# Performance work log

Measured on AMD Instinct MI355X. Metric: run time of the kernel, lower is better.

The kernel has to match this reference:

```python
import jax, jax.numpy as jnp
import numpy as np

N_NODES = 100000
N_EDGES = 1_600_000
D = 64


def setup_inputs() -> dict:
    key = jax.random.key(0)
    ks = jax.random.split(key, 10)
    features = jax.random.normal(ks[0], (N_NODES, D), dtype=jnp.float32)
    src = jax.random.randint(ks[1], (N_EDGES,), 0, N_NODES, dtype=jnp.int64)
    dst = jax.random.randint(ks[2], (N_EDGES,), 0, N_NODES, dtype=jnp.int64)
    s = 1.0 / np.sqrt(D)
    W0 = jax.random.uniform(ks[3], (D, D), jnp.float32, -s, s)
    b0 = jnp.zeros((D,), jnp.float32)
    W1 = jax.random.uniform(ks[4], (D, D), jnp.float32, -s, s)
    b1 = jnp.zeros((D,), jnp.float32)
    W2 = jax.random.uniform(ks[5], (D, D), jnp.float32, -s, s)
    b2 = jnp.zeros((D,), jnp.float32)
    return {"features": features, "src": src, "dst": dst,
            "W0": W0, "b0": b0, "W1": W1, "b1": b1, "W2": W2, "b2": b2}


def _graph_conv_left(h, src, dst, deg_inv, W, b, act):
    # norm='left': scale source features by 1/out_degree, then copy-sum aggregate
    h = h * deg_inv[:, None]          # [N, d]
    msgs = h[src]                     # [E, d] gather
    agg = jax.ops.segment_sum(msgs, dst, num_segments=N_NODES)  # [N, d]
    out = agg @ W + b
    return act(out) if act is not None else out


def reference(features, src, dst, W0, b0, W1, b1, W2, b2):
    # out-degree with clamp(min=1), as in DGL GraphConv
    deg = jax.ops.segment_sum(jnp.ones((N_EDGES,), jnp.float32), src,
                              num_segments=N_NODES)
    deg_inv = 1.0 / jnp.maximum(deg, 1.0)
    h = _graph_conv_left(features, src, dst, deg_inv, W0, b0, jax.nn.relu)
    h = _graph_conv_left(h, src, dst, deg_inv, W1, b1, jax.nn.relu)
    h = _graph_conv_left(h, src, dst, deg_inv, W2, b2, None)
    mN = jnp.mean(h, axis=0, keepdims=True)  # readout_nodes op='mean', single graph -> [1, d]
    return (h, mN)
```

## Files before the change

### kernel.cpp

```cpp
#include <hip/hip_runtime.h>
#include <hip/hip_fp16.h>

#define D 64
#define NBUK 391
#define NBIN (2 * NBUK)
#define CHUNK 8192
#define PBSTRIDE 256

__global__ __launch_bounds__(256) void phase1_kernel(const int* __restrict__ src,
                                                     const int* __restrict__ dst,
                                                     int* __restrict__ per_block, int E) {
    __shared__ int h[NBIN];
    int tid = (int)threadIdx.x;
    for (int j = tid; j < NBIN; j += 256) h[j] = 0;
    __syncthreads();
    int base = blockIdx.x * CHUNK;
    int cnt = min(CHUNK, E - base);
    for (int k = tid * 4; k < cnt; k += 1024) {
        if (k + 3 < cnt) {
            int4 d4 = *(const int4*)(dst + base + k);
            int4 s4 = *(const int4*)(src + base + k);
            atomicAdd(&h[d4.x >> 8], 1); atomicAdd(&h[d4.y >> 8], 1);
            atomicAdd(&h[d4.z >> 8], 1); atomicAdd(&h[d4.w >> 8], 1);
            atomicAdd(&h[NBUK + (s4.x >> 8)], 1); atomicAdd(&h[NBUK + (s4.y >> 8)], 1);
            atomicAdd(&h[NBUK + (s4.z >> 8)], 1); atomicAdd(&h[NBUK + (s4.w >> 8)], 1);
        } else {
            int kend = (k + 4 < cnt) ? k + 4 : cnt;
            for (int t = k; t < kend; ++t) {
                atomicAdd(&h[dst[base + t] >> 8], 1);
                atomicAdd(&h[NBUK + (src[base + t] >> 8)], 1);
            }
        }
    }
    __syncthreads();
    for (int j = tid; j < NBIN; j += 256) per_block[j * PBSTRIDE + blockIdx.x] = h[j];
}

__global__ __launch_bounds__(256) void scanA_kernel(int* __restrict__ per_block,
                                                    int* __restrict__ total) {
    int wv = (int)threadIdx.x >> 6;
    int lane = (int)threadIdx.x & 63;
    int j = blockIdx.x * 4 + wv;
    if (j >= NBIN) return;
    int* pb = per_block + (size_t)j * PBSTRIDE;
    int4 v = *(const int4*)(pb + lane * 4);
    int s1 = v.x + v.y, s2 = s1 + v.z, s3 = s2 + v.w;
    int x = s3;
#pragma unroll
    for (int d = 1; d < 64; d <<= 1) {
        int t = __shfl_up(x, d);
        if (lane >= d) x += t;
    }
    int excl = x - s3;
    int4 r = make_int4(excl, excl + v.x, excl + s1, excl + s2);
    *(int4*)(pb + lane * 4) = r;
    if (lane == 63) total[j] = x;
}

__global__ __launch_bounds__(512) void scanB_kernel(const int* __restrict__ total,
                                                    int* __restrict__ cb_dst,
                                                    int* __restrict__ cb_src,
                                                    float* __restrict__ msum) {
    __shared__ int s[512];
    int tid = (int)threadIdx.x;
    if (tid < D) msum[tid] = 0.0f;
    for (int half = 0; half < 2; ++half) {
        int v = (tid < NBUK) ? total[half * NBUK + tid] : 0;
        s[tid] = v;
        __syncthreads();
        for (int off = 1; off < 512; off <<= 1) {
            int t = (tid >= off) ? s[tid - off] : 0;
            __syncthreads();
            s[tid] += t;
            __syncthreads();
        }
        int* cb = half ? cb_src : cb_dst;
        if (tid < NBUK) cb[tid] = s[tid] - v;
        if (tid == NBUK - 1) cb[NBUK] = s[tid];
        __syncthreads();
    }
}

__global__ __launch_bounds__(256) void phase2_kernel(const int* __restrict__ src,
                                                     const int* __restrict__ dst,
                                                     const int* __restrict__ per_block,
                                                     const int* __restrict__ cb_dst,
                                                     const int* __restrict__ cb_src,
                                                     int* __restrict__ pairs,
                                                     unsigned char* __restrict__ skeys, int E) {
    __shared__ int lcur[NBIN];
    int tid = (int)threadIdx.x;
    for (int j = tid; j < NBIN; j += 256)
        lcur[j] = per_block[(size_t)j * PBSTRIDE + blockIdx.x] +
                  (j < NBUK ? cb_dst[j] : cb_src[j - NBUK]);
    __syncthreads();
    int base = blockIdx.x * CHUNK;
    int cnt = min(CHUNK, E - base);
    for (int k = tid * 4; k < cnt; k += 1024) {
        if (k + 3 < cnt) {
            int4 d4 = *(const int4*)(dst + base + k);
            int4 s4 = *(const int4*)(src + base + k);
            int p;
            p = atomicAdd(&lcur[d4.x >> 8], 1); pairs[p] = (s4.x << 8) | (d4.x & 255);
            p = atomicAdd(&lcur[d4.y >> 8], 1); pairs[p] = (s4.y << 8) | (d4.y & 255);
            p = atomicAdd(&lcur[d4.z >> 8], 1); pairs[p] = (s4.z << 8) | (d4.z & 255);
            p = atomicAdd(&lcur[d4.w >> 8], 1); pairs[p] = (s4.w << 8) | (d4.w & 255);
            p = atomicAdd(&lcur[NBUK + (s4.x >> 8)], 1); skeys[p] = (unsigned char)(s4.x & 255);
            p = atomicAdd(&lcur[NBUK + (s4.y >> 8)], 1); skeys[p] = (unsigned char)(s4.y & 255);
            p = atomicAdd(&lcur[NBUK + (s4.z >> 8)], 1); skeys[p] = (unsigned char)(s4.z & 255);
            p = atomicAdd(&lcur[NBUK + (s4.w >> 8)], 1); skeys[p] = (unsigned char)(s4.w & 255);
        } else {
            int kend = (k + 4 < cnt) ? k + 4 : cnt;
            for (int t = k; t < kend; ++t) {
                int dv = dst[base + t], sv = src[base + t];
                int p = atomicAdd(&lcur[dv >> 8], 1);
                pairs[p] = (sv << 8) | (dv & 255);
                p = atomicAdd(&lcur[NBUK + (sv >> 8)], 1);
                skeys[p] = (unsigned char)(sv & 255);
            }
        }
    }
}

__global__ __launch_bounds__(256) void finalize_csr_kernel(const int* __restrict__ pairs,
                                                           const unsigned char* __restrict__ skeys,
                                                           const int* __restrict__ cb_dst,
                                                           const int* __restrict__ cb_src,
                                                           const float* __restrict__ feat,
                                                           int* __restrict__ row_ptr,
                                                           int* __restrict__ col,
                                                           float* __restrict__ dinv,
                                                           __half* __restrict__ hs, int N) {
    __shared__ int fine[256];
    __shared__ int lcur[256];
    __shared__ float dsh[256];
    __shared__ int wtot[4], wexcl[4];
    int b = (int)blockIdx.x;
    int tid = (int)threadIdx.x, lane = tid & 63, wv = tid >> 6;
    int g = b * 256 + tid;

    fine[tid] = 0;
    __syncthreads();
    int sb0 = cb_src[b], sb1 = cb_src[b + 1];
    for (int i = sb0 + tid; i < sb1; i += 256) atomicAdd(&fine[skeys[i]], 1);
    __syncthreads();
    float dv_ = 1.0f / fmaxf((float)fine[tid], 1.0f);
    dsh[tid] = dv_;
    if (g < N) dinv[g] = dv_;
    __syncthreads();

    {
        int q = tid & 7;
        int rbase = tid >> 3;
        for (int p = 0; p < 8; ++p) {
            int r = p * 32 + rbase;
            int node = b * 256 + r;
            if (node < N) {
                float sc = dsh[r];
                const float4* f = (const float4*)(feat + (size_t)node * D + q * 8);
                float4 v0 = f[0], v1 = f[1];
                __half2 h[4];
                h[0] = __floats2half2_rn(v0.x * sc, v0.y * sc);
                h[1] = __floats2half2_rn(v0.z * sc, v0.w * sc);
                h[2] = __floats2half2_rn(v1.x * sc, v1.y * sc);
                h[3] = __floats2half2_rn(v1.z * sc, v1.w * sc);
                *(float4*)(hs + (size_t)node * D + q * 8) = *(float4*)h;
            }
        }
    }
    __syncthreads();

    fine[tid] = 0;
    __syncthreads();
    int cb0 = cb_dst[b], cb1 = cb_dst[b + 1];
    for (int i = cb0 + tid; i < cb1; i += 256) atomicAdd(&fine[pairs[i] & 255], 1);
    __syncthreads();
    int v = fine[tid], x = v;
#pragma unroll
    for (int d = 1; d < 64; d <<= 1) {
        int t = __shfl_up(x, d);
        if (lane >= d) x += t;
    }
    if (lane == 63) wtot[wv] = x;
    __syncthreads();
    if (tid == 0) {
        int a = 0;
#pragma unroll
        for (int k = 0; k < 4; ++k) { wexcl[k] = a; a += wtot[k]; }
    }
    __syncthreads();
    int excl = x - v + wexcl[wv];
    if (g <= N) row_ptr[g] = cb0 + excl;
    lcur[tid] = cb0 + excl;
    __syncthreads();
    for (int i = cb0 + tid; i < cb1; i += 256) {
        int p = pairs[i];
        int pos = atomicAdd(&lcur[p & 255], 1);
        col[pos] = p >> 8;
    }
}

__device__ inline void accum8(float* a, float4 raw) {
    __half2* h = (__half2*)&raw;
#pragma unroll
    for (int k = 0; k < 4; ++k) {
        float2 f = __half22float2(h[k]);
        a[2 * k] += f.x;
        a[2 * k + 1] += f.y;
    }
}

__global__ __launch_bounds__(256) void fused_kernel(const __half* __restrict__ hs_in,
                                                    const int* __restrict__ row_ptr,
                                                    const int* __restrict__ col,
                                                    const float* __restrict__ W,
                                                    const float* __restrict__ bias,
                                                    const float* __restrict__ dinv,
                                                    float* __restrict__ outf,
                                                    __half* __restrict__ outh,
                                                    float* __restrict__ msum,
                                                    int N, int mode) {
    int tid = (int)threadIdx.x;
    int lane = tid & 63;
    int wv = tid >> 6;
    int sg = lane >> 3;
    int q = lane & 7;
    int g = wv * 8 + sg;

    float Wreg[64];
#pragma unroll
    for (int k = 0; k < 64; ++k) Wreg[k] = W[k * 64 + lane];
    float breg = bias[lane];

    __shared__ float aggT[32][68];
    float colacc = 0.0f;

    int ntiles = (N + 31) >> 5;
    for (int tile = blockIdx.x; tile < ntiles; tile += gridDim.x) {
        int node_g = tile * 32 + g;
        float a[8];
#pragma unroll
        for (int k = 0; k < 8; ++k) a[k] = 0.0f;
        if (node_g < N) {
            int beg = row_ptr[node_g], end = row_ptr[node_g + 1];
            int j = beg;
            for (; j + 3 < end; j += 4) {
                int s0 = col[j], s1 = col[j + 1], s2 = col[j + 2], s3 = col[j + 3];
                float4 r0 = *(const float4*)(hs_in + (size_t)s0 * D + q * 8);
                float4 r1 = *(const float4*)(hs_in + (size_t)s1 * D + q * 8);
                float4 r2 = *(const float4*)(hs_in + (size_t)s2 * D + q * 8);
                float4 r3 = *(const float4*)(hs_in + (size_t)s3 * D + q * 8);
                accum8(a, r0); accum8(a, r1); accum8(a, r2); accum8(a, r3);
            }
            for (; j < end; ++j) {
                int s0 = col[j];
                float4 r0 = *(const float4*)(hs_in + (size_t)s0 * D + q * 8);
                accum8(a, r0);
            }
        }
        *(float4*)(&aggT[g][q * 8]) = make_float4(a[0], a[1], a[2], a[3]);
        *(float4*)(&aggT[g][q * 8 + 4]) = make_float4(a[4], a[5], a[6], a[7]);

#pragma unroll
        for (int rr = 0; rr < 8; ++rr) {
            int r = wv * 8 + rr;
            int node = tile * 32 + r;
            if (node < N) {
                float acc0 = breg, acc1 = 0.0f;
                const float4* Ar = (const float4*)(&aggT[r][0]);
#pragma unroll
                for (int k4 = 0; k4 < 16; k4 += 2) {
                    float4 av0 = Ar[k4];
                    float4 av1 = Ar[k4 + 1];
                    acc0 = fmaf(av0.x, Wreg[k4 * 4 + 0], acc0);
                    acc0 = fmaf(av0.y, Wreg[k4 * 4 + 1], acc0);
                    acc0 = fmaf(av0.z, Wreg[k4 * 4 + 2], acc0);
                    acc0 = fmaf(av0.w, Wreg[k4 * 4 + 3], acc0);
                    acc1 = fmaf(av1.x, Wreg[k4 * 4 + 4], acc1);
                    acc1 = fmaf(av1.y, Wreg[k4 * 4 + 5], acc1);
                    acc1 = fmaf(av1.z, Wreg[k4 * 4 + 6], acc1);
                    acc1 = fmaf(av1.w, Wreg[k4 * 4 + 7], acc1);
                }
                float acc = acc0 + acc1;
                if (mode == 0) {
                    acc = fmaxf(acc, 0.0f) * dinv[node];
                    outh[(size_t)node * D + lane] = __float2half(acc);
                } else {
                    colacc += acc;
                    outf[(size_t)node * D + lane] = acc;
                }
            }
        }
    }

    if (mode == 1) {
        __shared__ float red[256];
        red[tid] = colacc;
        __syncthreads();
        if (wv == 0) {
            float s = red[lane] + red[64 + lane] + red[128 + lane] + red[192 + lane];
            atomicAdd(&msum[lane], s);
        }
    }
}

__global__ void finalize_kernel(const float* __restrict__ msum, float* __restrict__ outMean,
                                float invN) {
    outMean[threadIdx.x] = msum[threadIdx.x] * invN;
}

extern "C" void kernel_launch(void* const* d_in, const int* in_sizes, int n_in,
                              void* d_out, int out_size, void* d_ws, size_t ws_size,
                              hipStream_t stream) {
    const float* feat = (const float*)d_in[0];
    const int* src = (const int*)d_in[1];
    const int* dst = (const int*)d_in[2];
    const float* W0 = (const float*)d_in[3];
    const float* b0 = (const float*)d_in[4];
    const float* W1 = (const float*)d_in[5];
    const float* b1 = (const float*)d_in[6];
    const float* W2 = (const float*)d_in[7];
    const float* b2 = (const float*)d_in[8];

    const int N = in_sizes[0] / D;
    const int E = in_sizes[1];
    float* out = (float*)d_out;

    const int NBLK = (E + CHUNK - 1) / CHUNK;

    int* wsi = (int*)d_ws;
    const size_t NA = 100352;
    int*   row_ptr  = wsi;
    float* dinv     = (float*)(wsi + NA);
    float* msum     = (float*)(wsi + 2 * NA);
    int*   total    = wsi + 2 * NA + 256;
    int*   cb_dst   = wsi + 2 * NA + 1280;
    int*   cb_src   = wsi + 2 * NA + 1792;
    int*   per_blk  = wsi + 2 * NA + 2304;
    int*   pairs    = wsi + 2 * NA + 203008;
    unsigned char* skeys = (unsigned char*)(pairs + (size_t)E);
    int*   col      = pairs + (size_t)E + 400000;
    __half* hsA     = (__half*)(col + (size_t)E);
    __half* hsB     = hsA + (size_t)N * D;

    hipMemsetAsync(per_blk, 0, sizeof(int) * (size_t)NBIN * PBSTRIDE, stream);

    phase1_kernel<<<NBLK, 256, 0, stream>>>(src, dst, per_blk, E);
    scanA_kernel<<<(NBIN + 3) / 4, 256, 0, stream>>>(per_blk, total);
    scanB_kernel<<<1, 512, 0, stream>>>(total, cb_dst, cb_src, msum);
    phase2_kernel<<<NBLK, 256, 0, stream>>>(src, dst, per_blk, cb_dst, cb_src, pairs, skeys, E);
    finalize_csr_kernel<<<NBUK, 256, 0, stream>>>(pairs, skeys, cb_dst, cb_src, feat,
                                                  row_ptr, col, dinv, hsA, N);

    const int FG = 1024;
    fused_kernel<<<FG, 256, 0, stream>>>(hsA, row_ptr, col, W0, b0, dinv, nullptr, hsB, msum, N, 0);
    fused_kernel<<<FG, 256, 0, stream>>>(hsB, row_ptr, col, W1, b1, dinv, nullptr, hsA, msum, N, 0);
    fused_kernel<<<FG, 256, 0, stream>>>(hsA, row_ptr, col, W2, b2, dinv, out, nullptr, msum, N, 1);

    finalize_kernel<<<1, 64, 0, stream>>>(msum, out + (size_t)N * D, 1.0f / (float)N);
}
```

Baseline: 324.8 us.

## Stage neighbor gathers via async global-to-LDS loads with double buffering

After: 307.9 us. 5.2% less time.

```diff
diff --git a/kernel.cpp b/kernel.cpp
--- a/kernel.cpp
+++ b/kernel.cpp
@@ -6,6 +6,15 @@
 #define NBIN (2 * NBUK)
 #define CHUNK 8192
 #define PBSTRIDE 256
+
+__device__ __forceinline__ void llds16(const void* g, const void* l) {
+    __builtin_amdgcn_global_load_lds((const __attribute__((address_space(1))) void*)g,
+                                     (__attribute__((address_space(3))) void*)l, 16, 0, 0);
+}
+__device__ __forceinline__ void llds4(const void* g, const void* l) {
+    __builtin_amdgcn_global_load_lds((const __attribute__((address_space(1))) void*)g,
+                                     (__attribute__((address_space(3))) void*)l, 4, 0, 0);
+}
 
 __global__ __launch_bounds__(256) void phase1_kernel(const int* __restrict__ src,
                                                      const int* __restrict__ dst,
@@ -37,13 +46,21 @@
 }
 
 __global__ __launch_bounds__(256) void scanA_kernel(int* __restrict__ per_block,
-                                                    int* __restrict__ total) {
+                                                    int* __restrict__ total, int nblk) {
     int wv = (int)threadIdx.x >> 6;
     int lane = (int)threadIdx.x & 63;
     int j = blockIdx.x * 4 + wv;
     if (j >= NBIN) return;
     int* pb = per_block + (size_t)j * PBSTRIDE;
-    int4 v = *(const int4*)(pb + lane * 4);
+    int idx = lane * 4;
+    int4 v = make_int4(0, 0, 0, 0);
+    if (idx + 3 < nblk) {
+        v = *(const int4*)(pb + idx);
+    } else if (idx < nblk) {
+        v.x = pb[idx];
+        if (idx + 1 < nblk) v.y = pb[idx + 1];
+        if (idx + 2 < nblk) v.z = pb[idx + 2];
+    }
     int s1 = v.x + v.y, s2 = s1 + v.z, s3 = s2 + v.w;
     int x = s3;
 #pragma unroll
@@ -53,7 +70,7 @@
     }
     int excl = x - s3;
     int4 r = make_int4(excl, excl + v.x, excl + s1, excl + s2);
-    *(int4*)(pb + lane * 4) = r;
+    *(int4*)(pb + idx) = r;
     if (lane == 63) total[j] = x;
 }
 
@@ -220,6 +237,7 @@
                                                     __half* __restrict__ outh,
                                                     float* __restrict__ msum,
                                                     int N, int mode) {
+    __shared__ __align__(16) unsigned char smem[39936];
     int tid = (int)threadIdx.x;
     int lane = tid & 63;
     int wv = tid >> 6;
@@ -227,47 +245,94 @@
     int q = lane & 7;
     int g = wv * 8 + sg;
 
+    unsigned char* wbase = smem + wv * 8192;
+    int* colsh = (int*)(smem + 32768 + wv * 1536);
+
     float Wreg[64];
 #pragma unroll
     for (int k = 0; k < 64; ++k) Wreg[k] = W[k * 64 + lane];
     float breg = bias[lane];
-
-    __shared__ float aggT[32][68];
     float colacc = 0.0f;
 
     int ntiles = (N + 31) >> 5;
     for (int tile = blockIdx.x; tile < ntiles; tile += gridDim.x) {
         int node_g = tile * 32 + g;
+        int beg = row_ptr[min(node_g, N)];
+        int end = row_ptr[min(node_g + 1, N)];
+        int deg = end - beg;
+
+        int wfirst = tile * 32 + wv * 8;
+        int cb = row_ptr[min(wfirst, N)];
+        int ce = row_ptr[min(wfirst + 8, N)];
+        int cnt = ce - cb;
+        int off = beg - cb;
+
+        int md = deg;
+        md = max(md, __shfl_xor(md, 8));
+        md = max(md, __shfl_xor(md, 16));
+        md = max(md, __shfl_xor(md, 32));
+        int rounds = (md + 3) >> 2;
+
         float a[8];
 #pragma unroll
         for (int k = 0; k < 8; ++k) a[k] = 0.0f;
-        if (node_g < N) {
-            int beg = row_ptr[node_g], end = row_ptr[node_g + 1];
-            int j = beg;
-            for (; j + 3 < end; j += 4) {
-                int s0 = col[j], s1 = col[j + 1], s2 = col[j + 2], s3 = col[j + 3];
-                float4 r0 = *(const float4*)(hs_in + (size_t)s0 * D + q * 8);
-                float4 r1 = *(const float4*)(hs_in + (size_t)s1 * D + q * 8);
-                float4 r2 = *(const float4*)(hs_in + (size_t)s2 * D + q * 8);
-                float4 r3 = *(const float4*)(hs_in + (size_t)s3 * D + q * 8);
-                accum8(a, r0); accum8(a, r1); accum8(a, r2); accum8(a, r3);
-            }
-            for (; j < end; ++j) {
+
+        if (cnt <= 384) {
+            for (int k = 0; k * 64 < cnt; ++k) {
+                int i = k * 64 + lane;
+                if (i < cnt) llds4(col + cb + i, (unsigned char*)colsh + k * 256);
+            }
+            asm volatile("s_waitcnt vmcnt(0)" ::: "memory");
+            __builtin_amdgcn_sched_barrier(0);
+
+            auto issue = [&](int b) {
+                unsigned char* buf = wbase + ((b & 1) << 12);
+#pragma unroll
+                for (int u = 0; u < 4; ++u) {
+                    int e = (b << 2) + u;
+                    if (e < deg) {
+                        int srcn = colsh[off + e];
+                        llds16(hs_in + (size_t)srcn * D + q * 8, buf + (u << 10));
+                    }
+                }
+            };
+            if (rounds > 0) issue(0);
+            if (rounds > 1) issue(1);
+            for (int b = 0; b < rounds; ++b) {
+                if (b + 1 < rounds) {
+                    asm volatile("s_waitcnt vmcnt(4)" ::: "memory");
+                } else {
+                    asm volatile("s_waitcnt vmcnt(0)" ::: "memory");
+                }
+                __builtin_amdgcn_sched_barrier(0);
+                unsigned char* buf = wbase + ((b & 1) << 12);
+#pragma unroll
+                for (int u = 0; u < 4; ++u) {
+                    int e = (b << 2) + u;
+                    if (e < deg) {
+                        float4 raw = *(const float4*)(buf + (u << 10) + lane * 16);
+                        accum8(a, raw);
+                    }
+                }
+                if (b + 2 < rounds) issue(b + 2);
+            }
+        } else {
+            for (int j = beg; j < end; ++j) {
                 int s0 = col[j];
                 float4 r0 = *(const float4*)(hs_in + (size_t)s0 * D + q * 8);
                 accum8(a, r0);
             }
         }
-        *(float4*)(&aggT[g][q * 8]) = make_float4(a[0], a[1], a[2], a[3]);
-        *(float4*)(&aggT[g][q * 8 + 4]) = make_float4(a[4], a[5], a[6], a[7]);
+
+        *(float4*)(wbase + sg * 272 + q * 32) = make_float4(a[0], a[1], a[2], a[3]);
+        *(float4*)(wbase + sg * 272 + q * 32 + 16) = make_float4(a[4], a[5], a[6], a[7]);
 
 #pragma unroll
         for (int rr = 0; rr < 8; ++rr) {
-            int r = wv * 8 + rr;
-            int node = tile * 32 + r;
+            int node = tile * 32 + wv * 8 + rr;
             if (node < N) {
                 float acc0 = breg, acc1 = 0.0f;
-                const float4* Ar = (const float4*)(&aggT[r][0]);
+                const float4* Ar = (const float4*)(wbase + rr * 272);
 #pragma unroll
                 for (int k4 = 0; k4 < 16; k4 += 2) {
                     float4 av0 = Ar[k4];
@@ -294,7 +359,7 @@
     }
 
     if (mode == 1) {
-        __shared__ float red[256];
+        float* red = (float*)(smem + 38912);
         red[tid] = colacc;
         __syncthreads();
         if (wv == 0) {
@@ -343,10 +408,9 @@
     __half* hsA     = (__half*)(col + (size_t)E);
     __half* hsB     = hsA + (size_t)N * D;
 
-    hipMemsetAsync(per_blk, 0, sizeof(int) * (size_t)NBIN * PBSTRIDE, stream);
 
     phase1_kernel<<<NBLK, 256, 0, stream>>>(src, dst, per_blk, E);
-    scanA_kernel<<<(NBIN + 3) / 4, 256, 0, stream>>>(per_blk, total);
+    scanA_kernel<<<(NBIN + 3) / 4, 256, 0, stream>>>(per_blk, total, NBLK);
     scanB_kernel<<<1, 512, 0, stream>>>(total, cb_dst, cb_src, msum);
     phase2_kernel<<<NBLK, 256, 0, stream>>>(src, dst, per_blk, cb_dst, cb_src, pairs, skeys, E);
     finalize_csr_kernel<<<NBUK, 256, 0, stream>>>(pairs, skeys, cb_dst, cb_src, feat,
```

## Prefetch next tile's column indices into LDS and software-pipeline gathers

Applied to the files above, without the earlier changes.

Result: no change. 319.9 us (-1.5%).

```diff
diff --git a/kernel.cpp b/kernel.cpp
--- a/kernel.cpp
+++ b/kernel.cpp
@@ -37,13 +37,21 @@
 }
 
 __global__ __launch_bounds__(256) void scanA_kernel(int* __restrict__ per_block,
-                                                    int* __restrict__ total) {
+                                                    int* __restrict__ total, int nblk) {
     int wv = (int)threadIdx.x >> 6;
     int lane = (int)threadIdx.x & 63;
     int j = blockIdx.x * 4 + wv;
     if (j >= NBIN) return;
     int* pb = per_block + (size_t)j * PBSTRIDE;
-    int4 v = *(const int4*)(pb + lane * 4);
+    int idx = lane * 4;
+    int4 v = make_int4(0, 0, 0, 0);
+    if (idx + 3 < nblk) {
+        v = *(const int4*)(pb + idx);
+    } else if (idx < nblk) {
+        v.x = pb[idx];
+        if (idx + 1 < nblk) v.y = pb[idx + 1];
+        if (idx + 2 < nblk) v.z = pb[idx + 2];
+    }
     int s1 = v.x + v.y, s2 = s1 + v.z, s3 = s2 + v.w;
     int x = s3;
 #pragma unroll
@@ -53,7 +61,7 @@
     }
     int excl = x - s3;
     int4 r = make_int4(excl, excl + v.x, excl + s1, excl + s2);
-    *(int4*)(pb + lane * 4) = r;
+    *(int4*)(pb + idx) = r;
     if (lane == 63) total[j] = x;
 }
 
@@ -210,16 +218,19 @@
     }
 }
 
-__global__ __launch_bounds__(256) void fused_kernel(const __half* __restrict__ hs_in,
-                                                    const int* __restrict__ row_ptr,
-                                                    const int* __restrict__ col,
-                                                    const float* __restrict__ W,
-                                                    const float* __restrict__ bias,
-                                                    const float* __restrict__ dinv,
-                                                    float* __restrict__ outf,
-                                                    __half* __restrict__ outh,
-                                                    float* __restrict__ msum,
-                                                    int N, int mode) {
+__global__ __launch_bounds__(256, 3) void fused_kernel(const __half* __restrict__ hs_in,
+                                                       const int* __restrict__ row_ptr,
+                                                       const int* __restrict__ col,
+                                                       const float* __restrict__ W,
+                                                       const float* __restrict__ bias,
+                                                       const float* __restrict__ dinv,
+                                                       float* __restrict__ outf,
+                                                       __half* __restrict__ outh,
+                                                       float* __restrict__ msum,
+                                                       int N, int mode) {
+    __shared__ int colsh[2][4][384];
+    __shared__ float aggT[32][68];
+    __shared__ float red[256];
     int tid = (int)threadIdx.x;
     int lane = tid & 63;
     int wv = tid >> 6;
@@ -231,33 +242,96 @@
 #pragma unroll
     for (int k = 0; k < 64; ++k) Wreg[k] = W[k * 64 + lane];
     float breg = bias[lane];
-
-    __shared__ float aggT[32][68];
     float colacc = 0.0f;
 
     int ntiles = (N + 31) >> 5;
-    for (int tile = blockIdx.x; tile < ntiles; tile += gridDim.x) {
-        int node_g = tile * 32 + g;
+    int tile = (int)blockIdx.x;
+
+    int beg, deg, off, cnt;
+    {
+        int node = tile * 32 + g;
+        beg = row_ptr[min(node, N)];
+        int end = row_ptr[min(node + 1, N)];
+        int cb = __shfl(beg, 0);
+        int ce = __shfl(end, 56);
+        cnt = ce - cb; off = beg - cb; deg = end - beg;
+        if (cnt <= 384) {
+#pragma unroll
+            for (int k = 0; k < 6; ++k) {
+                int i = k * 64 + lane;
+                if (i < cnt) colsh[0][wv][i] = col[cb + i];
+            }
+        }
+    }
+    int p = 0;
+
+    while (tile < ntiles) {
+        int md = deg;
+        md = max(md, __shfl_xor(md, 8));
+        md = max(md, __shfl_xor(md, 16));
+        md = max(md, __shfl_xor(md, 32));
+        int rounds = (md + 3) >> 2;
+
         float a[8];
 #pragma unroll
         for (int k = 0; k < 8; ++k) a[k] = 0.0f;
-        if (node_g < N) {
-            int beg = row_ptr[node_g], end = row_ptr[node_g + 1];
-            int j = beg;
-            for (; j + 3 < end; j += 4) {
-                int s0 = col[j], s1 = col[j + 1], s2 = col[j + 2], s3 = col[j + 3];
-                float4 r0 = *(const float4*)(hs_in + (size_t)s0 * D + q * 8);
-                float4 r1 = *(const float4*)(hs_in + (size_t)s1 * D + q * 8);
-                float4 r2 = *(const float4*)(hs_in + (size_t)s2 * D + q * 8);
-                float4 r3 = *(const float4*)(hs_in + (size_t)s3 * D + q * 8);
-                accum8(a, r0); accum8(a, r1); accum8(a, r2); accum8(a, r3);
-            }
-            for (; j < end; ++j) {
+
+        if (cnt <= 384) {
+            const int* cbuf = &colsh[p][wv][0];
+            int cl = cnt - 1;
+            float4 A0, A1, A2, A3, B0, B1, B2, B3;
+#define LD1(dstv, e_) { int ci = min(off + (e_), cl); int srcn = cbuf[ci]; \
+                        dstv = *(const float4*)(hs_in + (size_t)srcn * D + q * 8); }
+#define ISS(X0, X1, X2, X3, b_) { int eb = (b_) << 2; \
+        LD1(X0, eb) LD1(X1, eb + 1) LD1(X2, eb + 2) LD1(X3, eb + 3) }
+#define CNS(X0, X1, X2, X3, b_) { int eb = (b_) << 2; \
+        if (eb < deg) accum8(a, X0); if (eb + 1 < deg) accum8(a, X1); \
+        if (eb + 2 < deg) accum8(a, X2); if (eb + 3 < deg) accum8(a, X3); }
+            if (rounds > 0) {
+                ISS(A0, A1, A2, A3, 0)
+                if (rounds > 1) ISS(B0, B1, B2, B3, 1)
+                int b = 0;
+                while (true) {
+                    CNS(A0, A1, A2, A3, b)
+                    if (b + 2 < rounds) ISS(A0, A1, A2, A3, b + 2)
+                    ++b; if (b >= rounds) break;
+                    CNS(B0, B1, B2, B3, b)
+                    if (b + 2 < rounds) ISS(B0, B1, B2, B3, b + 2)
+                    ++b; if (b >= rounds) break;
+                }
+            }
+#undef LD1
+#undef ISS
+#undef CNS
+        } else {
+            int end = beg + deg;
+            for (int j = beg; j < end; ++j) {
                 int s0 = col[j];
                 float4 r0 = *(const float4*)(hs_in + (size_t)s0 * D + q * 8);
                 accum8(a, r0);
             }
         }
+
+        int tile2 = tile + (int)gridDim.x;
+        bool hn = tile2 < ntiles;
+        int beg2 = 0, deg2 = 0, off2 = 0, cnt2 = 0, cb2 = 0;
+        if (hn) {
+            int node2 = tile2 * 32 + g;
+            beg2 = row_ptr[min(node2, N)];
+            int end2 = row_ptr[min(node2 + 1, N)];
+            cb2 = __shfl(beg2, 0);
+            int ce2 = __shfl(end2, 56);
+            cnt2 = ce2 - cb2; off2 = beg2 - cb2; deg2 = end2 - beg2;
+        }
+        int stg[6];
+        bool sv[6];
+#pragma unroll
+        for (int k = 0; k < 6; ++k) {
+            int i = k * 64 + lane;
+            sv[k] = hn && cnt2 <= 384 && i < cnt2;
+            stg[k] = sv[k] ? col[cb2 + i] : 0;
+        }
+
         *(float4*)(&aggT[g][q * 8]) = make_float4(a[0], a[1], a[2], a[3]);
         *(float4*)(&aggT[g][q * 8 + 4]) = make_float4(a[4], a[5], a[6], a[7]);
 
@@ -291,10 +365,17 @@
                 }
             }
         }
+
+#pragma unroll
+        for (int k = 0; k < 6; ++k)
+            if (sv[k]) colsh[p ^ 1][wv][k * 64 + lane] = stg[k];
+
+        p ^= 1;
+        tile = tile2;
+        beg = beg2; deg = deg2; off = off2; cnt = cnt2;
     }
 
     if (mode == 1) {
-        __shared__ float red[256];
         red[tid] = colacc;
         __syncthreads();
         if (wv == 0) {
@@ -343,16 +424,14 @@
     __half* hsA     = (__half*)(col + (size_t)E);
     __half* hsB     = hsA + (size_t)N * D;
 
-    hipMemsetAsync(per_blk, 0, sizeof(int) * (size_t)NBIN * PBSTRIDE, stream);
-
     phase1_kernel<<<NBLK, 256, 0, stream>>>(src, dst, per_blk, E);
-    scanA_kernel<<<(NBIN + 3) / 4, 256, 0, stream>>>(per_blk, total);
+    scanA_kernel<<<(NBIN + 3) / 4, 256, 0, stream>>>(per_blk, total, NBLK);
     scanB_kernel<<<1, 512, 0, stream>>>(total, cb_dst, cb_src, msum);
     phase2_kernel<<<NBLK, 256, 0, stream>>>(src, dst, per_blk, cb_dst, cb_src, pairs, skeys, E);
     finalize_csr_kernel<<<NBUK, 256, 0, stream>>>(pairs, skeys, cb_dst, cb_src, feat,
                                                   row_ptr, col, dinv, hsA, N);
 
-    const int FG = 1024;
+    const int FG = 768;
     fused_kernel<<<FG, 256, 0, stream>>>(hsA, row_ptr, col, W0, b0, dinv, nullptr, hsB, msum, N, 0);
     fused_kernel<<<FG, 256, 0, stream>>>(hsB, row_ptr, col, W1, b1, dinv, nullptr, hsA, msum, N, 0);
     fused_kernel<<<FG, 256, 0, stream>>>(hsA, row_ptr, col, W2, b2, dinv, out, nullptr, msum, N, 1);
```
